# Performance work log

Measured on AMD Instinct MI355X. Metric: run time of the kernel, lower is better.

## Reference

```python
import jax, jax.numpy as jnp
import numpy as np

BLOCK_SIZE = 64
TOP_K = 4
D_MODEL = 256


def setup_inputs() -> dict:
    key = jax.random.key(0)
    kq, kk, kv = jax.random.split(key, 3)
    B, N, D = 4, 4096, D_MODEL
    q = jax.random.normal(kq, (B, N, D), dtype=jnp.float32)
    k = jax.random.normal(kk, (B, N, D), dtype=jnp.float32)
    v = jax.random.normal(kv, (B, N, D), dtype=jnp.float32)
    return {"q": q, "k": k, "v": v}


def _block_sparse_mask(q, k):
    # q, k: (B, N, D). Returns (B, N, N) bool mask (True = keep).
    B, N, D = q.shape
    nb = N // BLOCK_SIZE
    q_cent = q.reshape(B, nb, BLOCK_SIZE, D).mean(axis=2)  # (B, nb, D)
    k_cent = k.reshape(B, nb, BLOCK_SIZE, D).mean(axis=2)  # (B, nb, D)
    # pairwise Euclidean distance between centroids (nb is small: 64)
    diff = q_cent[:, :, None, :] - k_cent[:, None, :, :]   # (B, nb, nb, D)
    dist = jnp.sqrt(jnp.sum(diff * diff, axis=-1))          # (B, nb, nb)
    kk_ = min(TOP_K, nb)
    _, top_idx = jax.lax.top_k(-dist, kk_)                  # smallest distances
    mask = jnp.zeros((B, nb, nb), dtype=bool)
    b_idx = jnp.arange(B)[:, None, None]
    r_idx = jnp.arange(nb)[None, :, None]
    mask = mask.at[b_idx, r_idx, top_idx].set(True)
    # expand block mask to full (B, N, N) via broadcast-reshape
    mask_full = jnp.broadcast_to(
        mask[:, :, None, :, None], (B, nb, BLOCK_SIZE, nb, BLOCK_SIZE)
    ).reshape(B, N, N)
    return mask_full


def reference(q, k, v):
    mask = _block_sparse_mask(q, k)
    scale = 1.0 / (D_MODEL ** 0.5)
    scores = jnp.einsum('bqd,bkd->bqk', q, k) * scale       # (B, N, N)
    scores = jnp.where(mask, scores, -jnp.inf)
    attn = jax.nn.softmax(scores, axis=-1)
    out = jnp.einsum('bqk,bkd->bqd', attn, v)               # (B, N, D)
    return out
```

## Files before the change

kernel.cpp:

```cpp
#include <hip/hip_runtime.h>
#include <math.h>
#include <stdint.h>

#define BATCH 4
#define NSEQ 4096
#define DM 256
#define BLK 64
#define NB 64
#define TOPK 4

typedef unsigned short u16;
typedef unsigned int u32;
typedef __attribute__((ext_vector_type(8))) _Float16 f16x8;
typedef __attribute__((ext_vector_type(4))) float f32x4;

__device__ __forceinline__ u16 f2h(float f) {
    union { _Float16 h; u16 u; } c;
    c.h = (_Float16)f;
    return c.u;
}

__global__ __launch_bounds__(256) void prep_kernel(
    const float* __restrict__ q, const float* __restrict__ k, const float* __restrict__ v,
    u16* __restrict__ qf, u16* __restrict__ kf, u16* __restrict__ vtg,
    float* __restrict__ qc, float* __restrict__ kc)
{
    __shared__ u16 vt[256 * 66];
    const int gblk = blockIdx.x;
    const int d = threadIdx.x;
    const size_t base = (size_t)gblk * (BLK * DM);

    float s = 0.f;
#pragma unroll 8
    for (int r = 0; r < BLK; ++r) {
        float x = q[base + (size_t)r * DM + d];
        s += x;
        qf[base + (size_t)r * DM + d] = f2h(x);
    }
    qc[(size_t)gblk * DM + d] = s * (1.f / BLK);

    s = 0.f;
#pragma unroll 8
    for (int r = 0; r < BLK; ++r) {
        float x = k[base + (size_t)r * DM + d];
        s += x;
        kf[base + (size_t)r * DM + d] = f2h(x);
    }
    kc[(size_t)gblk * DM + d] = s * (1.f / BLK);

#pragma unroll 8
    for (int r = 0; r < BLK; ++r)
        vt[d * 66 + r] = f2h(v[base + (size_t)r * DM + d]);
    __syncthreads();

    const int w = threadIdx.x >> 6, lane = threadIdx.x & 63;
    const int half = lane >> 5, c = lane & 31;
    const u32* vts = (const u32*)vt;
    u32* vo = (u32*)vtg + (base >> 1);
#pragma unroll
    for (int i = 0; i < 32; ++i) {
        int dr = w * 64 + i * 2 + half;
        vo[dr * 32 + c] = vts[dr * 33 + c];
    }
}

__global__ __launch_bounds__(256) void topk_kernel(const float* __restrict__ qc,
                                                   const float* __restrict__ kc,
                                                   int* __restrict__ top4)
{
    extern __shared__ float kcl[];
    float* red = kcl + 64 * 258;
    const int bid = blockIdx.x;
    const int swz = (bid & 7) * 32 + (bid >> 3);
    const int b = swz >> 6;
    const int t = threadIdx.x;

    const float* kcb = kc + (size_t)(b * NB) * DM;
#pragma unroll
    for (int it = 0; it < 64; ++it) {
        int li = t + it * 256;
        kcl[(li >> 8) * 258 + (li & 255)] = kcb[li];
    }
    __syncthreads();

    const int j = t & 63, dq = t >> 6;
    const float* qrow = qc + (size_t)swz * DM;
    float s = 0.f;
#pragma unroll 8
    for (int dd = 0; dd < 64; ++dd) {
        float diff = qrow[dq * 64 + dd] - kcl[j * 258 + dq * 64 + dd];
        s += diff * diff;
    }
    red[dq * 64 + j] = s;
    __syncthreads();

    if (t < 64) {
        float dist = sqrtf(red[t] + red[64 + t] + red[128 + t] + red[192 + t]);
        for (int sel = 0; sel < TOPK; ++sel) {
            float mv = dist;
            int mi = t;
#pragma unroll
            for (int off = 32; off >= 1; off >>= 1) {
                float ov = __shfl_xor(mv, off);
                int oi = __shfl_xor(mi, off);
                if (ov < mv || (ov == mv && oi < mi)) { mv = ov; mi = oi; }
            }
            if (t == 0) top4[swz * 4 + sel] = mi;
            if (t == mi) dist = 3.0e38f;
        }
    }
}

#define KQ_O 16896
#define VT_O 16896

__global__ __launch_bounds__(256, 2) void attn_kernel(
    const u16* __restrict__ qf, const u16* __restrict__ kf,
    const u16* __restrict__ vtg, const int* __restrict__ top4, float* __restrict__ out)
{
    extern __shared__ u16 smem[];
    const int bid = blockIdx.x;
    const int swz = (bid & 7) * 32 + (bid >> 3);
    const int b = swz >> 6, qb = swz & 63;
    const int tid = threadIdx.x;
    const int w = tid >> 6, lane = tid & 63;
    const int x = lane & 15, g = lane >> 4;

    auto stage64 = [&](int dsthw, const u16* __restrict__ src) {
#pragma unroll
        for (int it = 0; it < 8; ++it) {
            int li = tid + it * 256;
            int row = li >> 5, c8 = li & 31;
            *(uint4*)&smem[dsthw + row * 264 + c8 * 8] = *(const uint4*)&src[row * 256 + c8 * 8];
        }
    };
    auto stageVt = [&](const u16* __restrict__ src) {
#pragma unroll
        for (int it = 0; it < 8; ++it) {
            int li = tid + it * 256;
            int dr = li >> 3, c8 = li & 7;
            *(uint4*)&smem[VT_O + dr * 64 + (c8 ^ (dr & 7)) * 8] = *(const uint4*)&src[dr * 64 + c8 * 8];
        }
    };

    int sel[TOPK];
#pragma unroll
    for (int t = 0; t < TOPK; ++t) sel[t] = top4[swz * 4 + t];

    const size_t qbase = (size_t)swz * (BLK * DM);
    stage64(0, qf + qbase);
    stage64(KQ_O, kf + (size_t)(b * NB + sel[0]) * (BLK * DM));
    __syncthreads();

    f16x8 bq[8];
    const int qrow = w * 16 + x;
#pragma unroll
    for (int dc = 0; dc < 8; ++dc)
        bq[dc] = *(const f16x8*)&smem[qrow * 264 + dc * 32 + g * 8];

    f32x4 S[16];
#pragma unroll
    for (int t = 0; t < 16; ++t) S[t] = (f32x4){0.f, 0.f, 0.f, 0.f};

#pragma unroll
    for (int kb = 0; kb < TOPK; ++kb) {
#pragma unroll
        for (int jt = 0; jt < 4; ++jt) {
            f32x4 acc = S[kb * 4 + jt];
#pragma unroll
            for (int dc = 0; dc < 8; ++dc) {
                f16x8 ak = *(const f16x8*)&smem[KQ_O + (jt * 16 + x) * 264 + dc * 32 + g * 8];
                acc = __builtin_amdgcn_mfma_f32_16x16x32_f16(ak, bq[dc], acc, 0, 0, 0);
            }
            S[kb * 4 + jt] = acc;
        }
        __syncthreads();
        if (kb < TOPK - 1) {
            stage64(KQ_O, kf + (size_t)(b * NB + sel[kb + 1]) * (BLK * DM));
            __syncthreads();
        }
    }

    float mx = -3.0e38f;
#pragma unroll
    for (int t = 0; t < 16; ++t)
#pragma unroll
        for (int r = 0; r < 4; ++r) { S[t][r] *= 0.0625f; mx = fmaxf(mx, S[t][r]); }
    mx = fmaxf(mx, __shfl_xor(mx, 16));
    mx = fmaxf(mx, __shfl_xor(mx, 32));
    float sum = 0.f;
#pragma unroll
    for (int t = 0; t < 16; ++t)
#pragma unroll
        for (int r = 0; r < 4; ++r) { float p = __expf(S[t][r] - mx); S[t][r] = p; sum += p; }
    sum += __shfl_xor(sum, 16);
    sum += __shfl_xor(sum, 32);
    const float inv = 1.f / sum;

    stageVt(vtg + (size_t)(b * NB + sel[0]) * (BLK * DM));
    u32* pw = (u32*)smem;
#pragma unroll
    for (int t = 0; t < 16; ++t)
#pragma unroll
        for (int rp = 0; rp < 2; ++rp) {
            u32 dw = (u32)f2h(S[t][2 * rp] * inv) | ((u32)f2h(S[t][2 * rp + 1] * inv) << 16);
            pw[qrow * 132 + t * 8 + g * 2 + rp] = dw;
        }
    __syncthreads();

    f32x4 O[16];
#pragma unroll
    for (int t = 0; t < 16; ++t) O[t] = (f32x4){0.f, 0.f, 0.f, 0.f};

#pragma unroll
    for (int kb = 0; kb < TOPK; ++kb) {
#pragma unroll
        for (int jc = 0; jc < 2; ++jc) {
            f16x8 pa = *(const f16x8*)&smem[qrow * 264 + kb * 64 + jc * 32 + g * 8];
#pragma unroll
            for (int dt = 0; dt < 16; ++dt) {
                f16x8 bv = *(const f16x8*)&smem[VT_O + (dt * 16 + x) * 64 + ((jc * 4 + g) ^ (x & 7)) * 8];
                O[dt] = __builtin_amdgcn_mfma_f32_16x16x32_f16(pa, bv, O[dt], 0, 0, 0);
            }
        }
        __syncthreads();
        if (kb < TOPK - 1) {
            stageVt(vtg + (size_t)(b * NB + sel[kb + 1]) * (BLK * DM));
            __syncthreads();
        }
    }

    float* ob = out + ((size_t)b * NSEQ + (size_t)qb * BLK) * DM;
#pragma unroll
    for (int dt = 0; dt < 16; ++dt)
#pragma unroll
        for (int r = 0; r < 4; ++r)
            ob[(size_t)(w * 16 + g * 4 + r) * DM + dt * 16 + x] = O[dt][r];
}

extern "C" void kernel_launch(void* const* d_in, const int* in_sizes, int n_in,
                              void* d_out, int out_size, void* d_ws, size_t ws_size,
                              hipStream_t stream) {
    const float* q = (const float*)d_in[0];
    const float* k = (const float*)d_in[1];
    const float* v = (const float*)d_in[2];
    float* out = (float*)d_out;

    const size_t nelem = (size_t)BATCH * NSEQ * DM;
    u16* qf = (u16*)d_ws;
    u16* kf = qf + nelem;
    u16* vtg = kf + nelem;
    float* qc = (float*)(vtg + nelem);
    float* kc = qc + (size_t)BATCH * NB * DM;
    int* top4 = (int*)(kc + (size_t)BATCH * NB * DM);

    prep_kernel<<<BATCH * NB, 256, 0, stream>>>(q, k, v, qf, kf, vtg, qc, kc);

    const int tk_lds = (64 * 258 + 256) * (int)sizeof(float);
    hipFuncSetAttribute((const void*)topk_kernel, hipFuncAttributeMaxDynamicSharedMemorySize, tk_lds);
    topk_kernel<<<BATCH * NB, 256, tk_lds, stream>>>(qc, kc, top4);

    const int at_lds = 33792 * 2;
    hipFuncSetAttribute((const void*)attn_kernel, hipFuncAttributeMaxDynamicSharedMemorySize, at_lds);
    attn_kernel<<<BATCH * NB, 256, at_lds, stream>>>(qf, kf, vtg, top4, out);
}
```

Measured before the change: 121.7 us.

## Fuse top-k centroid selection into attention kernel and read K/V directly from global

Removes the separate top-k kernel launch by computing centroid distances and top-4 selection inside each attention block, using wave-level shuffle reductions. K and V^T tiles are now read straight from global memory into MFMA operands instead of being staged through LDS with barriers. This cuts LDS use, allowing three blocks per CU. The trade-off is redundant centroid-distance work per block and uncoalesced, cache-dependent global loads feeding the MFMAs.

```diff
diff --git a/kernel.cpp b/kernel.cpp
--- a/kernel.cpp
+++ b/kernel.cpp
@@ -64,99 +64,57 @@
     }
 }
 
-__global__ __launch_bounds__(256) void topk_kernel(const float* __restrict__ qc,
-                                                   const float* __restrict__ kc,
-                                                   int* __restrict__ top4)
-{
-    extern __shared__ float kcl[];
-    float* red = kcl + 64 * 258;
-    const int bid = blockIdx.x;
-    const int swz = (bid & 7) * 32 + (bid >> 3);
-    const int b = swz >> 6;
-    const int t = threadIdx.x;
-
-    const float* kcb = kc + (size_t)(b * NB) * DM;
-#pragma unroll
-    for (int it = 0; it < 64; ++it) {
-        int li = t + it * 256;
-        kcl[(li >> 8) * 258 + (li & 255)] = kcb[li];
-    }
-    __syncthreads();
-
-    const int j = t & 63, dq = t >> 6;
-    const float* qrow = qc + (size_t)swz * DM;
-    float s = 0.f;
-#pragma unroll 8
-    for (int dd = 0; dd < 64; ++dd) {
-        float diff = qrow[dq * 64 + dd] - kcl[j * 258 + dq * 64 + dd];
-        s += diff * diff;
-    }
-    red[dq * 64 + j] = s;
-    __syncthreads();
-
-    if (t < 64) {
-        float dist = sqrtf(red[t] + red[64 + t] + red[128 + t] + red[192 + t]);
-        for (int sel = 0; sel < TOPK; ++sel) {
-            float mv = dist;
-            int mi = t;
-#pragma unroll
-            for (int off = 32; off >= 1; off >>= 1) {
-                float ov = __shfl_xor(mv, off);
-                int oi = __shfl_xor(mi, off);
-                if (ov < mv || (ov == mv && oi < mi)) { mv = ov; mi = oi; }
-            }
-            if (t == 0) top4[swz * 4 + sel] = mi;
-            if (t == mi) dist = 3.0e38f;
-        }
-    }
-}
-
-#define KQ_O 16896
-#define VT_O 16896
-
-__global__ __launch_bounds__(256, 2) void attn_kernel(
-    const u16* __restrict__ qf, const u16* __restrict__ kf,
-    const u16* __restrict__ vtg, const int* __restrict__ top4, float* __restrict__ out)
+__global__ __launch_bounds__(256, 3) void attn_kernel(
+    const u16* __restrict__ qf, const u16* __restrict__ kf, const u16* __restrict__ vtg,
+    const float* __restrict__ qc, const float* __restrict__ kc, float* __restrict__ out)
 {
     extern __shared__ u16 smem[];
+    float* red = (float*)&smem[64 * 264];
     const int bid = blockIdx.x;
     const int swz = (bid & 7) * 32 + (bid >> 3);
     const int b = swz >> 6, qb = swz & 63;
     const int tid = threadIdx.x;
     const int w = tid >> 6, lane = tid & 63;
     const int x = lane & 15, g = lane >> 4;
-
-    auto stage64 = [&](int dsthw, const u16* __restrict__ src) {
-#pragma unroll
-        for (int it = 0; it < 8; ++it) {
-            int li = tid + it * 256;
-            int row = li >> 5, c8 = li & 31;
-            *(uint4*)&smem[dsthw + row * 264 + c8 * 8] = *(const uint4*)&src[row * 256 + c8 * 8];
-        }
-    };
-    auto stageVt = [&](const u16* __restrict__ src) {
-#pragma unroll
-        for (int it = 0; it < 8; ++it) {
-            int li = tid + it * 256;
-            int dr = li >> 3, c8 = li & 7;
-            *(uint4*)&smem[VT_O + dr * 64 + (c8 ^ (dr & 7)) * 8] = *(const uint4*)&src[dr * 64 + c8 * 8];
-        }
-    };
+    const int qrow = w * 16 + x;
+
+    const u16* qfb = qf + (size_t)swz * (BLK * DM);
+    f16x8 bq[8];
+#pragma unroll
+    for (int dc = 0; dc < 8; ++dc)
+        bq[dc] = *(const f16x8*)&qfb[qrow * 256 + dc * 32 + g * 8];
+
+    const float* qcp = qc + (size_t)swz * DM;
+    const float* kcb = kc + (size_t)(b * NB) * DM;
+    f32x4 qcv = *(const f32x4*)(qcp + lane * 4);
+#pragma unroll
+    for (int jj = 0; jj < 16; ++jj) {
+        int j = w * 16 + jj;
+        f32x4 kcv = *(const f32x4*)(kcb + (size_t)j * DM + lane * 4);
+        f32x4 df = qcv - kcv;
+        float s = df.x * df.x + df.y * df.y + df.z * df.z + df.w * df.w;
+#pragma unroll
+        for (int off = 32; off >= 1; off >>= 1) s += __shfl_xor(s, off);
+        if (lane == 0) red[j] = s;
+    }
+    __syncthreads();
 
     int sel[TOPK];
-#pragma unroll
-    for (int t = 0; t < TOPK; ++t) sel[t] = top4[swz * 4 + t];
-
-    const size_t qbase = (size_t)swz * (BLK * DM);
-    stage64(0, qf + qbase);
-    stage64(KQ_O, kf + (size_t)(b * NB + sel[0]) * (BLK * DM));
-    __syncthreads();
-
-    f16x8 bq[8];
-    const int qrow = w * 16 + x;
-#pragma unroll
-    for (int dc = 0; dc < 8; ++dc)
-        bq[dc] = *(const f16x8*)&smem[qrow * 264 + dc * 32 + g * 8];
+    {
+        float dval = red[lane];
+        for (int t = 0; t < TOPK; ++t) {
+            float mv = dval;
+            int mi = lane;
+#pragma unroll
+            for (int off = 32; off >= 1; off >>= 1) {
+                float ov = __shfl_xor(mv, off);
+                int oi = __shfl_xor(mi, off);
+                if (ov < mv || (ov == mv && oi < mi)) { mv = ov; mi = oi; }
+            }
+            sel[t] = mi;
+            if (lane == mi) dval = 3.0e38f;
+        }
+    }
 
     f32x4 S[16];
 #pragma unroll
@@ -164,20 +122,16 @@
 
 #pragma unroll
     for (int kb = 0; kb < TOPK; ++kb) {
+        const u16* kfb = kf + (size_t)(b * NB + sel[kb]) * (BLK * DM);
 #pragma unroll
         for (int jt = 0; jt < 4; ++jt) {
             f32x4 acc = S[kb * 4 + jt];
 #pragma unroll
             for (int dc = 0; dc < 8; ++dc) {
-                f16x8 ak = *(const f16x8*)&smem[KQ_O + (jt * 16 + x) * 264 + dc * 32 + g * 8];
+                f16x8 ak = *(const f16x8*)&kfb[(jt * 16 + x) * 256 + dc * 32 + g * 8];
                 acc = __builtin_amdgcn_mfma_f32_16x16x32_f16(ak, bq[dc], acc, 0, 0, 0);
             }
             S[kb * 4 + jt] = acc;
-        }
-        __syncthreads();
-        if (kb < TOPK - 1) {
-            stage64(KQ_O, kf + (size_t)(b * NB + sel[kb + 1]) * (BLK * DM));
-            __syncthreads();
         }
     }
 
@@ -197,7 +151,6 @@
     sum += __shfl_xor(sum, 32);
     const float inv = 1.f / sum;
 
-    stageVt(vtg + (size_t)(b * NB + sel[0]) * (BLK * DM));
     u32* pw = (u32*)smem;
 #pragma unroll
     for (int t = 0; t < 16; ++t)
@@ -214,19 +167,15 @@
 
 #pragma unroll
     for (int kb = 0; kb < TOPK; ++kb) {
+        const u16* vtb = vtg + (size_t)(b * NB + sel[kb]) * (BLK * DM);
 #pragma unroll
         for (int jc = 0; jc < 2; ++jc) {
             f16x8 pa = *(const f16x8*)&smem[qrow * 264 + kb * 64 + jc * 32 + g * 8];
 #pragma unroll
             for (int dt = 0; dt < 16; ++dt) {
-                f16x8 bv = *(const f16x8*)&smem[VT_O + (dt * 16 + x) * 64 + ((jc * 4 + g) ^ (x & 7)) * 8];
+                f16x8 bv = *(const f16x8*)&vtb[(dt * 16 + x) * 64 + jc * 32 + g * 8];
                 O[dt] = __builtin_amdgcn_mfma_f32_16x16x32_f16(pa, bv, O[dt], 0, 0, 0);
             }
-        }
-        __syncthreads();
-        if (kb < TOPK - 1) {
-            stageVt(vtg + (size_t)(b * NB + sel[kb + 1]) * (BLK * DM));
-            __syncthreads();
         }
     }
 
@@ -252,15 +201,10 @@
     u16* vtg = kf + nelem;
     float* qc = (float*)(vtg + nelem);
     float* kc = qc + (size_t)BATCH * NB * DM;
-    int* top4 = (int*)(kc + (size_t)BATCH * NB * DM);
 
     prep_kernel<<<BATCH * NB, 256, 0, stream>>>(q, k, v, qf, kf, vtg, qc, kc);
 
-    const int tk_lds = (64 * 258 + 256) * (int)sizeof(float);
-    hipFuncSetAttribute((const void*)topk_kernel, hipFuncAttributeMaxDynamicSharedMemorySize, tk_lds);
-    topk_kernel<<<BATCH * NB, 256, tk_lds, stream>>>(qc, kc, top4);
-
-    const int at_lds = 33792 * 2;
+    const int at_lds = 64 * 264 * 2 + 64 * 4;
     hipFuncSetAttribute((const void*)attn_kernel, hipFuncAttributeMaxDynamicSharedMemorySize, at_lds);
-    attn_kernel<<<BATCH * NB, 256, at_lds, stream>>>(qf, kf, vtg, top4, out);
-}
+    attn_kernel<<<BATCH * NB, 256, at_lds, stream>>>(qf, kf, vtg, qc, kc, out);
+}
```

Measured after the change: 154.0 us. 26.5% more time.
